# Kernel tuning notes

Measured on AMD Instinct MI355X. Metric: run time of the kernel, lower is better.

The kernel has to match this reference:

```python
import jax, jax.numpy as jnp
import numpy as np

CONV_NUM = 8
CONV_SIZE = 96
HIDDEN = 768  # = CONV_NUM * CONV_SIZE
MAX_LEN = 128


def get_entity(x, s, e):
    # x: [B, L, H]; mean of x[i, s[i]:max(e[i], s[i]+1)] per sample (ragged gather+mean)
    e = jnp.maximum(e, s + 1)
    pos = jnp.arange(x.shape[1])  # [L]
    mask = (pos[None, :] >= s[:, None]) & (pos[None, :] < e[:, None])  # [B, L]
    m = mask.astype(x.dtype)
    return jnp.einsum('blh,bl->bh', x, m) / jnp.sum(m, axis=1, keepdims=True)


def feature_abstract(head_ent, tail_ent, x, fc_W, fc_b):
    # head_ent/tail_ent: [B, HIDDEN] -> per-sample conv filters; x: [B, HIDDEN]
    B = x.shape[0]
    wh = head_ent.reshape(B * CONV_NUM, 1, 1, CONV_SIZE)
    wt = tail_ent.reshape(B * CONV_NUM, 1, 1, CONV_SIZE)
    lhs = x.reshape(1, B, 1, HIDDEN)  # NCHW, groups=B -> per-sample correlation
    h = jax.nn.relu(jax.lax.conv_general_dilated(lhs, wh, (1, 1), 'VALID', feature_group_count=B))
    t = jax.nn.relu(jax.lax.conv_general_dilated(lhs, wt, (1, 1), 'VALID', feature_group_count=B))
    # h,t: [1, B*CONV_NUM, 1, T] with T = HIDDEN - CONV_SIZE + 1
    ht = jnp.concatenate([h, t], axis=3).reshape(B * CONV_NUM, -1)  # [B*cn, 2T]
    ht = ht.reshape(B * CONV_NUM, -1, 2).mean(axis=-1)  # AvgPool1d(k=2, s=2) -> [B*cn, T]
    flat = ht.reshape(B, -1)  # [B, cn*T] (dropout is identity in eval)
    return flat @ fc_W.T + fc_b  # [B, HIDDEN]


def setup_inputs() -> dict:
    key = jax.random.key(0)
    ks = jax.random.split(key, 16)
    Bs, Bq, L, H = 400, 1200, MAX_LEN, HIDDEN

    def spans(k1, k2, B):
        s = jax.random.randint(k1, (B,), 0, 100)
        e = jnp.minimum(s + jax.random.randint(k2, (B,), 1, 20), L)
        return s.astype(jnp.int64), e.astype(jnp.int64)

    s_eh, s_eh_end = spans(ks[0], ks[1], Bs)
    s_et, s_et_end = spans(ks[2], ks[3], Bs)
    q_eh, q_eh_end = spans(ks[4], ks[5], Bq)
    q_et, q_et_end = spans(ks[6], ks[7], Bq)
    fc_in = (H - CONV_SIZE + 1) * CONV_NUM  # 5384
    return {
        'all_support': jax.random.normal(ks[8], (Bs, L, H), jnp.float32),
        'support_emb': jax.random.normal(ks[9], (Bs, H), jnp.float32),
        'all_query': jax.random.normal(ks[10], (Bq, L, H), jnp.float32),
        'query_emb': jax.random.normal(ks[11], (Bq, H), jnp.float32),
        'fc_W': jax.random.normal(ks[12], (H, fc_in), jnp.float32) / np.sqrt(fc_in),
        'fc_b': jnp.zeros((H,), jnp.float32),
        's_eh': s_eh, 's_eh_end': s_eh_end, 's_et': s_et, 's_et_end': s_et_end,
        'q_eh': q_eh, 'q_eh_end': q_eh_end, 'q_et': q_et, 'q_et_end': q_et_end,
        'N': 10, 'K': 5, 'total_Q': 150,
    }


def reference(all_support, support_emb, all_query, query_emb, fc_W, fc_b,
              s_eh, s_eh_end, s_et, s_et_end, q_eh, q_eh_end, q_et, q_et_end,
              N, K, total_Q):
    sh = get_entity(all_support, s_eh, s_eh_end)
    st = get_entity(all_support, s_et, s_et_end)
    qh = get_entity(all_query, q_eh, q_eh_end)
    qt = get_entity(all_query, q_et, q_et_end)

    sup = feature_abstract(sh, st, support_emb, fc_W, fc_b).reshape(-1, N, K, HIDDEN)
    qry = feature_abstract(qh, qt, query_emb, fc_W, fc_b).reshape(-1, total_Q, HIDDEN)

    proto = sup.mean(axis=2)  # [Be, N, H]
    # -||proto - query||^2 over feature dim -> [Be, total_Q, N]
    diff = proto[:, None, :, :] - qry[:, :, None, :]
    logits = -jnp.sum(diff * diff, axis=-1)
    minn = logits.min(axis=-1)
    logits = jnp.concatenate([logits, minn[..., None] - 1.0], axis=2)  # [Be, total_Q, N+1]
    pred = jnp.argmax(logits.reshape(-1, N + 1), axis=1)
    return logits, pred
```

## Files before the change

kernel.cpp:

```cpp
#include <hip/hip_runtime.h>

#define H        768
#define LMAX     128
#define CONV_NUM 8
#define CONV_SIZE 96
#define T_CONV   673
#define FC_IN    5384
#define KP       5408
#define KSTEPS   (KP / 32)
#define N_WAY    10
#define K_SHOT   5
#define TOTAL_Q  150
#define SPLITK   8
#define BS       400
#define BQ       1200
#define MTOT     1600
#define NPROTO   80
#define MA       1280

using s16x8 = __attribute__((ext_vector_type(8))) short;
using f32x4 = __attribute__((ext_vector_type(4))) float;
typedef unsigned short u16;

__device__ __forceinline__ u16 f2bf(float x) {
    unsigned u = __float_as_uint(x);
    u += 0x7FFFu + ((u >> 16) & 1u);
    return (u16)(u >> 16);
}
__device__ __forceinline__ float bf2f(u16 b) { return __uint_as_float(((unsigned)b) << 16); }

__device__ __forceinline__ void gl16(const u16* g, u16* l) {
    __builtin_amdgcn_global_load_lds(
        (const __attribute__((address_space(1))) unsigned int*)g,
        (__attribute__((address_space(3))) unsigned int*)l, 16, 0, 0);
}

#define HTS 678
#define XCS 784
__global__ __launch_bounds__(256, 4) void pre_kernel(
    const float* __restrict__ all_support, const float* __restrict__ all_query,
    const float* __restrict__ support_emb, const float* __restrict__ query_emb,
    const float* __restrict__ fc_W,
    const int* __restrict__ s_eh, const int* __restrict__ s_eh_end,
    const int* __restrict__ s_et, const int* __restrict__ s_et_end,
    const int* __restrict__ q_eh, const int* __restrict__ q_eh_end,
    const int* __restrict__ q_et, const int* __restrict__ q_et_end,
    u16* __restrict__ flatS, u16* __restrict__ A_bf,
    u16* __restrict__ Wh)
{
    int bid = blockIdx.x;
    int tid = threadIdx.x;

    if (bid >= MTOT) {
        int r = bid - MTOT;
        const float* wr = fc_W + (size_t)r * FC_IN;
        u16* whr = Wh + (size_t)r * KP;
        for (int j4 = tid; j4 < KP / 4; j4 += 256) {
            int j = j4 * 4;
            ushort4 o;
            if (j4 < FC_IN / 4) {
                float4 v = *(const float4*)(wr + j);
                o.x = f2bf(v.x); o.y = f2bf(v.y); o.z = f2bf(v.z); o.w = f2bf(v.w);
            } else {
                o.x = 0; o.y = 0; o.z = 0; o.w = 0;
            }
            *(ushort4*)(whr + j) = o;
        }
        return;
    }

    __shared__ u16 htb[16 * HTS];
    __shared__ u16 filt_h[16 * 96];
    __shared__ u16 filt_l[16 * 96];
    __shared__ u16 xcs[8][XCS];

    int b = bid;
    const float* src;
    int sh, eh, st, et;
    if (b < BS) {
        src = all_support + (size_t)b * LMAX * H;
        sh = s_eh[b]; eh = s_eh_end[b]; st = s_et[b]; et = s_et_end[b];
    } else {
        int m = b - BS;
        src = all_query + (size_t)m * LMAX * H;
        sh = q_eh[m]; eh = q_eh_end[m]; st = q_et[m]; et = q_et_end[m];
    }
    if (eh < sh + 1) eh = sh + 1;
    if (et < st + 1) et = st + 1;

    {
        float a0 = 0.f, a1 = 0.f, a2 = 0.f, b0 = 0.f, b1 = 0.f, b2 = 0.f;
        int r = sh;
        for (; r + 2 <= eh; r += 2) {
            const float* p0 = src + (size_t)r * H;
            const float* p1 = p0 + H;
            a0 += p0[tid]; a1 += p0[tid + 256]; a2 += p0[tid + 512];
            b0 += p1[tid]; b1 += p1[tid + 256]; b2 += p1[tid + 512];
        }
        if (r < eh) {
            const float* p0 = src + (size_t)r * H;
            a0 += p0[tid]; a1 += p0[tid + 256]; a2 += p0[tid + 512];
        }
        float rc = 1.0f / (float)(eh - sh);
        float m0 = (a0 + b0) * rc, m1 = (a1 + b1) * rc, m2 = (a2 + b2) * rc;
        u16 h0 = f2bf(m0), h1 = f2bf(m1), h2 = f2bf(m2);
        filt_h[tid] = h0;       filt_l[tid] = f2bf(m0 - bf2f(h0));
        filt_h[tid + 256] = h1; filt_l[tid + 256] = f2bf(m1 - bf2f(h1));
        filt_h[tid + 512] = h2; filt_l[tid + 512] = f2bf(m2 - bf2f(h2));
        a0 = a1 = a2 = b0 = b1 = b2 = 0.f;
        r = st;
        for (; r + 2 <= et; r += 2) {
            const float* p0 = src + (size_t)r * H;
            const float* p1 = p0 + H;
            a0 += p0[tid]; a1 += p0[tid + 256]; a2 += p0[tid + 512];
            b0 += p1[tid]; b1 += p1[tid + 256]; b2 += p1[tid + 512];
        }
        if (r < et) {
            const float* p0 = src + (size_t)r * H;
            a0 += p0[tid]; a1 += p0[tid + 256]; a2 += p0[tid + 512];
        }
        rc = 1.0f / (float)(et - st);
        m0 = (a0 + b0) * rc; m1 = (a1 + b1) * rc; m2 = (a2 + b2) * rc;
        h0 = f2bf(m0); h1 = f2bf(m1); h2 = f2bf(m2);
        filt_h[tid + 768] = h0;  filt_l[tid + 768] = f2bf(m0 - bf2f(h0));
        filt_h[tid + 1024] = h1; filt_l[tid + 1024] = f2bf(m1 - bf2f(h1));
        filt_h[tid + 1280] = h2; filt_l[tid + 1280] = f2bf(m2 - bf2f(h2));
    }

    {
        if (tid < 192) {
            int row = tid / 24, idx = tid % 24;
            int j = 768 - row + idx;
            if (j < XCS) xcs[row][j] = 0;
        }
        const float* xsrc = (b < BS) ? (support_emb + (size_t)b * H)
                                     : (query_emb + (size_t)(b - BS) * H);
        if (tid < 192) {
            float4 v = *(const float4*)(xsrc + tid * 4);
            u16 h[4] = {f2bf(v.x), f2bf(v.y), f2bf(v.z), f2bf(v.w)};
            #pragma unroll
            for (int u = 0; u < 4; ++u) {
                int i = tid * 4 + u;
                #pragma unroll
                for (int c = 0; c < 8; ++c)
                    if (i >= c) xcs[c][i - c] = h[u];
            }
        }
    }
    __syncthreads();

    {
        int lane = tid & 63, wv = tid >> 6;
        int n = lane & 15, g = lane >> 4;
        int afo = n * 96 + g * 8;
        s16x8 fh0 = *(const s16x8*)&filt_h[afo];
        s16x8 fh1 = *(const s16x8*)&filt_h[afo + 32];
        s16x8 fh2 = *(const s16x8*)&filt_h[afo + 64];
        s16x8 fl0 = *(const s16x8*)&filt_l[afo];
        s16x8 fl1 = *(const s16x8*)&filt_l[afo + 32];
        s16x8 fl2 = *(const s16x8*)&filt_l[afo + 64];
        const u16* xrow = &xcs[n & 7][g * 8 + (n & 8)];
        #pragma unroll 1
        for (int nt = wv; nt < 43; nt += 4) {
            const u16* xp = xrow + nt * 16;
            s16x8 x0 = *(const s16x8*)(xp);
            s16x8 x1 = *(const s16x8*)(xp + 32);
            s16x8 x2 = *(const s16x8*)(xp + 64);
            f32x4 a = (f32x4){0.f, 0.f, 0.f, 0.f};
            a = __builtin_amdgcn_mfma_f32_16x16x32_bf16(fh0, x0, a, 0, 0, 0);
            a = __builtin_amdgcn_mfma_f32_16x16x32_bf16(fl0, x0, a, 0, 0, 0);
            a = __builtin_amdgcn_mfma_f32_16x16x32_bf16(fh1, x1, a, 0, 0, 0);
            a = __builtin_amdgcn_mfma_f32_16x16x32_bf16(fl1, x1, a, 0, 0, 0);
            a = __builtin_amdgcn_mfma_f32_16x16x32_bf16(fh2, x2, a, 0, 0, 0);
            a = __builtin_amdgcn_mfma_f32_16x16x32_bf16(fl2, x2, a, 0, 0, 0);
            int pcol = nt * 16 + n;
            if (pcol < T_CONV) {
                #pragma unroll
                for (int r = 0; r < 4; ++r)
                    htb[(g * 4 + r) * HTS + pcol] = f2bf(fmaxf(a[r], 0.f));
            }
        }
    }
    __syncthreads();

    u16* oh = (b < BS) ? (flatS + (size_t)b * KP)
                       : (A_bf + (size_t)(NPROTO + b - BS) * KP);
    for (int f = 0; f < CONV_NUM; ++f) {
        for (int j = tid; j < T_CONV; j += 256) {
            int i0 = 2 * j, i1 = 2 * j + 1;
            float v0 = bf2f((i0 < T_CONV) ? htb[f * HTS + i0]
                                          : htb[(8 + f) * HTS + (i0 - T_CONV)]);
            float v1 = bf2f((i1 < T_CONV) ? htb[f * HTS + i1]
                                          : htb[(8 + f) * HTS + (i1 - T_CONV)]);
            oh[f * T_CONV + j] = f2bf(0.5f * (v0 + v1));
        }
    }
    for (int j = FC_IN + tid; j < KP; j += 256) oh[j] = 0;
}

__global__ __launch_bounds__(256) void avg_kernel(
    const u16* __restrict__ flatS, u16* __restrict__ A_bf)
{
    int i = blockIdx.x;
    size_t base = (size_t)i * K_SHOT * KP;
    for (int t = threadIdx.x; t < KP / 8; t += 256) {
        int j = t * 8;
        float s[8] = {0.f, 0.f, 0.f, 0.f, 0.f, 0.f, 0.f, 0.f};
        #pragma unroll
        for (int k = 0; k < K_SHOT; ++k) {
            s16x8 vh = *(const s16x8*)(flatS + base + (size_t)k * KP + j);
            #pragma unroll
            for (int u = 0; u < 8; ++u)
                s[u] += bf2f((u16)vh[u]);
        }
        s16x8 oh;
        #pragma unroll
        for (int u = 0; u < 8; ++u)
            oh[u] = (short)f2bf(s[u] * (1.0f / K_SHOT));
        *(s16x8*)(A_bf + (size_t)i * KP + j) = oh;
    }
}

#define ASEG 8192
#define BSEG 4096
#define BUFU (ASEG + BSEG)

#define STAGE(ks, buf) do {                                     \
    int kb_ = (ks) * 32;                                        \
    u16* L_ = &lds[buf][0];                                     \
    gl16(Ah_g + aoff0 + kb_, L_ + cA0 * 8);                     \
    gl16(Ah_g + aoff1 + kb_, L_ + cA1 * 8);                     \
    gl16(Ah_g + aoff2 + kb_, L_ + cA2 * 8);                     \
    gl16(Ah_g + aoff3 + kb_, L_ + cA3 * 8);                     \
    gl16(Bh_g + boff0 + kb_, L_ + ASEG + cB0 * 8);              \
    gl16(Bh_g + boff1 + kb_, L_ + ASEG + cB1 * 8);              \
} while (0)

__global__ __launch_bounds__(256, 2) void gemm_mfma(
    const u16* __restrict__ Ah_g, const u16* __restrict__ Bh_g,
    u16* __restrict__ partsB)
{
    __shared__ u16 lds[2][BUFU];

    int tid = threadIdx.x;
    int wg = (blockIdx.x & 7) * 30 + (blockIdx.x >> 3);
    int sk = wg / 30;
    int rem = wg % 30;
    int n0 = (rem / 5) * 128;
    int m0 = (rem % 5) * 256;

    int ks0 = (KSTEPS * sk) / SPLITK;
    int nk = (KSTEPS * (sk + 1)) / SPLITK - ks0;

    int cA0 = tid, cA1 = tid + 256, cA2 = tid + 512, cA3 = tid + 768;
    int cB0 = tid, cB1 = tid + 256;
    size_t aoff0 = (size_t)(m0 + (cA0 >> 6) * 16 + (cA0 & 15)) * KP + ((cA0 >> 4) & 3) * 8;
    size_t aoff1 = (size_t)(m0 + (cA1 >> 6) * 16 + (cA1 & 15)) * KP + ((cA1 >> 4) & 3) * 8;
    size_t aoff2 = (size_t)(m0 + (cA2 >> 6) * 16 + (cA2 & 15)) * KP + ((cA2 >> 4) & 3) * 8;
    size_t aoff3 = (size_t)(m0 + (cA3 >> 6) * 16 + (cA3 & 15)) * KP + ((cA3 >> 4) & 3) * 8;
    size_t boff0 = (size_t)(n0 + (cB0 >> 6) * 16 + (cB0 & 15)) * KP + ((cB0 >> 4) & 3) * 8;
    size_t boff1 = (size_t)(n0 + (cB1 >> 6) * 16 + (cB1 & 15)) * KP + ((cB1 >> 4) & 3) * 8;

    int w = tid >> 6, lane = tid & 63;
    int lfr = ((lane >> 4) * 16 + (lane & 15)) * 8;

    f32x4 acc[4][8];
    #pragma unroll
    for (int i = 0; i < 4; ++i)
        #pragma unroll
        for (int j = 0; j < 8; ++j) acc[i][j] = (f32x4){0.f, 0.f, 0.f, 0.f};

    STAGE(ks0, 0);
    STAGE(ks0 + 1, 1);

    int cur = 0;
    for (int k = 0; k < nk; ++k) {
        if (k + 1 < nk) asm volatile("s_waitcnt vmcnt(6)" ::: "memory");
        else            asm volatile("s_waitcnt vmcnt(0)" ::: "memory");
        __builtin_amdgcn_s_barrier();

        const u16* L = &lds[cur][0];
        s16x8 ah[4], bh[8];
        #pragma unroll
        for (int f = 0; f < 4; ++f)
            ah[f] = *(const s16x8*)(L + (w * 4 + f) * 512 + lfr);
        #pragma unroll
        for (int j = 0; j < 8; ++j)
            bh[j] = *(const s16x8*)(L + ASEG + j * 512 + lfr);
        asm volatile("s_waitcnt lgkmcnt(0)" ::: "memory");
        __builtin_amdgcn_s_barrier();

        if (k + 2 < nk) STAGE(ks0 + k + 2, cur);

        #pragma unroll
        for (int i = 0; i < 4; ++i)
            #pragma unroll
            for (int j = 0; j < 8; ++j)
                acc[i][j] = __builtin_amdgcn_mfma_f32_16x16x32_bf16(ah[i], bh[j], acc[i][j], 0, 0, 0);
        cur ^= 1;
    }

    int rbase = m0 + w * 64 + (lane >> 4) * 4;
    int cbase = n0 + (lane & 15);
    #pragma unroll
    for (int i = 0; i < 4; ++i) {
        int row0 = rbase + i * 16;
        #pragma unroll
        for (int j = 0; j < 8; ++j) {
            int col = cbase + j * 16;
            u16* dst = partsB + ((size_t)sk * MA + row0) * H + col;
            #pragma unroll
            for (int r = 0; r < 4; ++r)
                dst[(size_t)r * H] = f2bf(acc[i][j][r]);
        }
    }
}

__global__ __launch_bounds__(256) void protofin_kernel(
    const u16* __restrict__ partsB, float* __restrict__ proto)
{
    int i = blockIdx.x;
    int tid = threadIdx.x;
    #pragma unroll
    for (int q = 0; q < 3; ++q) {
        int d = tid + q * 256;
        float s = 0.f;
        #pragma unroll
        for (int sp = 0; sp < SPLITK; ++sp)
            s += bf2f(partsB[((size_t)sp * MA + i) * H + d]);
        proto[(size_t)i * H + d] = s;
    }
}

__global__ __launch_bounds__(256) void dist_kernel(
    const u16* __restrict__ partsB, const float* __restrict__ proto,
    float* __restrict__ outp)
{
    int bid = blockIdx.x;
    int e = bid / TOTAL_Q;
    int tid = threadIdx.x;
    int m = NPROTO + bid;
    int d0 = tid * 4;

    float qv0 = 0.f, qv1 = 0.f, qv2 = 0.f, qv3 = 0.f;
    if (tid < 192) {
        #pragma unroll
        for (int sp = 0; sp < SPLITK; ++sp) {
            ushort4 v = *(const ushort4*)(partsB + ((size_t)sp * MA + m) * H + d0);
            qv0 += bf2f(v.x); qv1 += bf2f(v.y); qv2 += bf2f(v.z); qv3 += bf2f(v.w);
        }
    }

    __shared__ float red[N_WAY][4];
    __shared__ float lvals[N_WAY];
    int wave = tid >> 6, lane = tid & 63;
    for (int n = 0; n < N_WAY; ++n) {
        float p = 0.f;
        if (tid < 192) {
            const float* pr = proto + (size_t)(e * N_WAY + n) * H + d0;
            float4 pv = *(const float4*)pr;
            float df0 = pv.x - qv0, df1 = pv.y - qv1, df2 = pv.z - qv2, df3 = pv.w - qv3;
            p = df0 * df0;
            p = fmaf(df1, df1, p);
            p = fmaf(df2, df2, p);
            p = fmaf(df3, df3, p);
        }
        #pragma unroll
        for (int off = 32; off > 0; off >>= 1)
            p += __shfl_down(p, off);
        if (lane == 0) red[n][wave] = p;
    }
    __syncthreads();
    if (tid < N_WAY) {
        float v = red[tid][0] + red[tid][1] + red[tid][2] + red[tid][3];
        lvals[tid] = -v;
        outp[(size_t)bid * (N_WAY + 1) + tid] = -v;
    }
    __syncthreads();
    if (tid == 0) {
        float mn = lvals[0];
        #pragma unroll
        for (int n = 1; n < N_WAY; ++n) mn = fminf(mn, lvals[n]);
        float last = mn - 1.0f;
        outp[(size_t)bid * (N_WAY + 1) + N_WAY] = last;
        float best = lvals[0];
        int bi = 0;
        for (int n = 1; n < N_WAY; ++n)
            if (lvals[n] > best) { best = lvals[n]; bi = n; }
        if (last > best) bi = N_WAY;
        outp[(size_t)BQ * (N_WAY + 1) + bid] = (float)bi;
    }
}

extern "C" void kernel_launch(void* const* d_in, const int* in_sizes, int n_in,
                              void* d_out, int out_size, void* d_ws, size_t ws_size,
                              hipStream_t stream)
{
    const float* all_support = (const float*)d_in[0];
    const float* support_emb = (const float*)d_in[1];
    const float* all_query   = (const float*)d_in[2];
    const float* query_emb   = (const float*)d_in[3];
    const float* fc_W        = (const float*)d_in[4];
    const int* s_eh     = (const int*)d_in[6];
    const int* s_eh_end = (const int*)d_in[7];
    const int* s_et     = (const int*)d_in[8];
    const int* s_et_end = (const int*)d_in[9];
    const int* q_eh     = (const int*)d_in[10];
    const int* q_eh_end = (const int*)d_in[11];
    const int* q_et     = (const int*)d_in[12];
    const int* q_et_end = (const int*)d_in[13];

    u16* partsB  = (u16*)d_ws;
    float* proto = (float*)(partsB + (size_t)SPLITK * MA * H);
    u16* Wh      = (u16*)(proto + (size_t)NPROTO * H);
    u16* A_bf    = Wh + (size_t)H * KP;
    u16* flatS   = A_bf + (size_t)MA * KP;

    pre_kernel<<<MTOT + H, 256, 0, stream>>>(
        all_support, all_query, support_emb, query_emb, fc_W,
        s_eh, s_eh_end, s_et, s_et_end, q_eh, q_eh_end, q_et, q_et_end,
        flatS, A_bf, Wh);

    avg_kernel<<<NPROTO, 256, 0, stream>>>(flatS, A_bf);

    gemm_mfma<<<240, 256, 0, stream>>>(A_bf, Wh, partsB);

    protofin_kernel<<<NPROTO, 256, 0, stream>>>(partsB, proto);

    dist_kernel<<<BQ, 256, 0, stream>>>(partsB, proto, (float*)d_out);
}
```

Before: 69.77 us.

## Vectorize pooled output stores, unroll span sums, widen avg and protofin kernels

The span-sum loops now unroll by four rows with more independent accumulators, so more loads are in flight per thread. The avg-pool output is written as 16-byte vectors, using a multiply-shift division to find the filter index, and the padding columns of the staging buffer are zeroed. avg_kernel is split across four y-blocks with one vector per thread, and protofin uses ushort4 loads with float4 stores. Together these target memory-bound tails in several stages, at the cost of more register use and extra per-element index arithmetic in the pooling step.

```diff
diff --git a/kernel.cpp b/kernel.cpp
--- a/kernel.cpp
+++ b/kernel.cpp
@@ -90,37 +90,50 @@
 
     {
         float a0 = 0.f, a1 = 0.f, a2 = 0.f, b0 = 0.f, b1 = 0.f, b2 = 0.f;
+        float c0 = 0.f, c1 = 0.f, c2 = 0.f, d0 = 0.f, d1 = 0.f, d2 = 0.f;
         int r = sh;
-        for (; r + 2 <= eh; r += 2) {
+        for (; r + 4 <= eh; r += 4) {
             const float* p0 = src + (size_t)r * H;
             const float* p1 = p0 + H;
+            const float* p2 = p0 + 2 * H;
+            const float* p3 = p0 + 3 * H;
             a0 += p0[tid]; a1 += p0[tid + 256]; a2 += p0[tid + 512];
             b0 += p1[tid]; b1 += p1[tid + 256]; b2 += p1[tid + 512];
-        }
-        if (r < eh) {
+            c0 += p2[tid]; c1 += p2[tid + 256]; c2 += p2[tid + 512];
+            d0 += p3[tid]; d1 += p3[tid + 256]; d2 += p3[tid + 512];
+        }
+        for (; r < eh; ++r) {
             const float* p0 = src + (size_t)r * H;
             a0 += p0[tid]; a1 += p0[tid + 256]; a2 += p0[tid + 512];
         }
         float rc = 1.0f / (float)(eh - sh);
-        float m0 = (a0 + b0) * rc, m1 = (a1 + b1) * rc, m2 = (a2 + b2) * rc;
+        float m0 = ((a0 + b0) + (c0 + d0)) * rc;
+        float m1 = ((a1 + b1) + (c1 + d1)) * rc;
+        float m2 = ((a2 + b2) + (c2 + d2)) * rc;
         u16 h0 = f2bf(m0), h1 = f2bf(m1), h2 = f2bf(m2);
         filt_h[tid] = h0;       filt_l[tid] = f2bf(m0 - bf2f(h0));
         filt_h[tid + 256] = h1; filt_l[tid + 256] = f2bf(m1 - bf2f(h1));
         filt_h[tid + 512] = h2; filt_l[tid + 512] = f2bf(m2 - bf2f(h2));
-        a0 = a1 = a2 = b0 = b1 = b2 = 0.f;
+        a0 = a1 = a2 = b0 = b1 = b2 = c0 = c1 = c2 = d0 = d1 = d2 = 0.f;
         r = st;
-        for (; r + 2 <= et; r += 2) {
+        for (; r + 4 <= et; r += 4) {
             const float* p0 = src + (size_t)r * H;
             const float* p1 = p0 + H;
+            const float* p2 = p0 + 2 * H;
+            const float* p3 = p0 + 3 * H;
             a0 += p0[tid]; a1 += p0[tid + 256]; a2 += p0[tid + 512];
             b0 += p1[tid]; b1 += p1[tid + 256]; b2 += p1[tid + 512];
-        }
-        if (r < et) {
+            c0 += p2[tid]; c1 += p2[tid + 256]; c2 += p2[tid + 512];
+            d0 += p3[tid]; d1 += p3[tid + 256]; d2 += p3[tid + 512];
+        }
+        for (; r < et; ++r) {
             const float* p0 = src + (size_t)r * H;
             a0 += p0[tid]; a1 += p0[tid + 256]; a2 += p0[tid + 512];
         }
         rc = 1.0f / (float)(et - st);
-        m0 = (a0 + b0) * rc; m1 = (a1 + b1) * rc; m2 = (a2 + b2) * rc;
+        m0 = ((a0 + b0) + (c0 + d0)) * rc;
+        m1 = ((a1 + b1) + (c1 + d1)) * rc;
+        m2 = ((a2 + b2) + (c2 + d2)) * rc;
         h0 = f2bf(m0); h1 = f2bf(m1); h2 = f2bf(m2);
         filt_h[tid + 768] = h0;  filt_l[tid + 768] = f2bf(m0 - bf2f(h0));
         filt_h[tid + 1024] = h1; filt_l[tid + 1024] = f2bf(m1 - bf2f(h1));
@@ -132,6 +145,10 @@
             int row = tid / 24, idx = tid % 24;
             int j = 768 - row + idx;
             if (j < XCS) xcs[row][j] = 0;
+        }
+        if (tid >= 192 && tid < 192 + 80) {
+            int t = tid - 192;
+            htb[(t / 5) * HTS + 673 + (t % 5)] = 0;
         }
         const float* xsrc = (b < BS) ? (support_emb + (size_t)b * H)
                                      : (query_emb + (size_t)(b - BS) * H);
@@ -185,40 +202,52 @@
 
     u16* oh = (b < BS) ? (flatS + (size_t)b * KP)
                        : (A_bf + (size_t)(NPROTO + b - BS) * KP);
-    for (int f = 0; f < CONV_NUM; ++f) {
-        for (int j = tid; j < T_CONV; j += 256) {
-            int i0 = 2 * j, i1 = 2 * j + 1;
-            float v0 = bf2f((i0 < T_CONV) ? htb[f * HTS + i0]
-                                          : htb[(8 + f) * HTS + (i0 - T_CONV)]);
-            float v1 = bf2f((i1 < T_CONV) ? htb[f * HTS + i1]
-                                          : htb[(8 + f) * HTS + (i1 - T_CONV)]);
-            oh[f * T_CONV + j] = f2bf(0.5f * (v0 + v1));
-        }
-    }
-    for (int j = FC_IN + tid; j < KP; j += 256) oh[j] = 0;
+    for (int t = tid; t < KP / 8; t += 256) {
+        int i0 = t * 8;
+        s16x8 o;
+        if (i0 < FC_IN) {
+            #pragma unroll
+            for (int u = 0; u < 8; ++u) {
+                int i = i0 + u;
+                int f = (int)(((unsigned)i * 24929u) >> 24);
+                int j = i - f * 673;
+                int e0 = 2 * j, e1 = 2 * j + 1;
+                float v0 = bf2f((e0 < T_CONV) ? htb[f * HTS + e0]
+                                              : htb[(8 + f) * HTS + (e0 - T_CONV)]);
+                float v1 = bf2f((e1 < T_CONV) ? htb[f * HTS + e1]
+                                              : htb[(8 + f) * HTS + (e1 - T_CONV)]);
+                o[u] = (short)f2bf(0.5f * (v0 + v1));
+            }
+        } else {
+            #pragma unroll
+            for (int u = 0; u < 8; ++u) o[u] = 0;
+        }
+        *(s16x8*)(oh + i0) = o;
+    }
 }
 
 __global__ __launch_bounds__(256) void avg_kernel(
     const u16* __restrict__ flatS, u16* __restrict__ A_bf)
 {
     int i = blockIdx.x;
+    int q = blockIdx.y;
     size_t base = (size_t)i * K_SHOT * KP;
-    for (int t = threadIdx.x; t < KP / 8; t += 256) {
-        int j = t * 8;
-        float s[8] = {0.f, 0.f, 0.f, 0.f, 0.f, 0.f, 0.f, 0.f};
-        #pragma unroll
-        for (int k = 0; k < K_SHOT; ++k) {
-            s16x8 vh = *(const s16x8*)(flatS + base + (size_t)k * KP + j);
-            #pragma unroll
-            for (int u = 0; u < 8; ++u)
-                s[u] += bf2f((u16)vh[u]);
-        }
-        s16x8 oh;
+    int t = threadIdx.x;
+    if (t >= 169) return;
+    int j = (q * 169 + t) * 8;
+    float s[8] = {0.f, 0.f, 0.f, 0.f, 0.f, 0.f, 0.f, 0.f};
+    #pragma unroll
+    for (int k = 0; k < K_SHOT; ++k) {
+        s16x8 vh = *(const s16x8*)(flatS + base + (size_t)k * KP + j);
         #pragma unroll
         for (int u = 0; u < 8; ++u)
-            oh[u] = (short)f2bf(s[u] * (1.0f / K_SHOT));
-        *(s16x8*)(A_bf + (size_t)i * KP + j) = oh;
-    }
+            s[u] += bf2f((u16)vh[u]);
+    }
+    s16x8 oh;
+    #pragma unroll
+    for (int u = 0; u < 8; ++u)
+        oh[u] = (short)f2bf(s[u] * (1.0f / K_SHOT));
+    *(s16x8*)(A_bf + (size_t)i * KP + j) = oh;
 }
 
 #define ASEG 8192
@@ -321,15 +350,15 @@
 {
     int i = blockIdx.x;
     int tid = threadIdx.x;
+    if (tid >= 192) return;
+    int d0 = tid * 4;
+    float s0 = 0.f, s1 = 0.f, s2 = 0.f, s3 = 0.f;
     #pragma unroll
-    for (int q = 0; q < 3; ++q) {
-        int d = tid + q * 256;
-        float s = 0.f;
-        #pragma unroll
-        for (int sp = 0; sp < SPLITK; ++sp)
-            s += bf2f(partsB[((size_t)sp * MA + i) * H + d]);
-        proto[(size_t)i * H + d] = s;
-    }
+    for (int sp = 0; sp < SPLITK; ++sp) {
+        ushort4 v = *(const ushort4*)(partsB + ((size_t)sp * MA + i) * H + d0);
+        s0 += bf2f(v.x); s1 += bf2f(v.y); s2 += bf2f(v.z); s3 += bf2f(v.w);
+    }
+    *(float4*)(proto + (size_t)i * H + d0) = make_float4(s0, s1, s2, s3);
 }
 
 __global__ __launch_bounds__(256) void dist_kernel(
@@ -421,7 +450,7 @@
         s_eh, s_eh_end, s_et, s_et_end, q_eh, q_eh_end, q_et, q_et_end,
         flatS, A_bf, Wh);
 
-    avg_kernel<<<NPROTO, 256, 0, stream>>>(flatS, A_bf);
+    avg_kernel<<<dim3(NPROTO, 4), 256, 0, stream>>>(flatS, A_bf);
 
     gemm_mfma<<<240, 256, 0, stream>>>(A_bf, Wh, partsB);
 
```

After: 69.57 us. Within noise of the previous version (-0.3%).
